# Performance work log

Hardware: AMD Instinct MI355X
Metric: run time of the kernel (lower is better)

The kernel has to match this reference:

```python
import jax, jax.numpy as jnp
import numpy as np


def setup_inputs() -> dict:
    key = jax.random.key(0)
    ks = jax.random.split(key, 5)
    B, S, D, F, E = 4, 4096, 512, 2048, 8
    scale = 0.02
    return {
        "x": jax.random.normal(ks[0], (B, S, D), dtype=jnp.float32),
        "gate_w": jax.random.normal(ks[1], (E, D), dtype=jnp.float32) * scale,
        "w1": jax.random.normal(ks[2], (E, F, D), dtype=jnp.float32) * scale,
        "w2": jax.random.normal(ks[3], (E, D, F), dtype=jnp.float32) * scale,
        "w3": jax.random.normal(ks[4], (E, F, D), dtype=jnp.float32) * scale,
        "top_k": 2,
    }


def _moe(x, gate_w, w1, w2, w3, top_k):
    B, S, D = x.shape
    E = gate_w.shape[0]
    xt = x.reshape(-1, D)                       # [T, D], T = B*S
    T = xt.shape[0]

    # --- router: softmax in float32, top-k, renormalize (matches Mixtral) ---
    logits = xt @ gate_w.T                      # [T, E]
    probs = jax.nn.softmax(logits.astype(jnp.float32), axis=-1)
    rw, sel = jax.lax.top_k(probs, top_k)       # [T, k], [T, k]
    rw = rw / jnp.sum(rw, axis=-1, keepdims=True)
    rw = rw.astype(x.dtype)

    # dense combine weights [T, E]: zero for unselected experts
    combine = jnp.zeros((T, E), dtype=x.dtype)
    combine = combine.at[jnp.arange(T)[:, None], sel].add(rw)

    # --- per-expert SwiGLU-style FFN (relu gate), combined by routing weights ---
    out = jnp.zeros_like(xt)
    for e in range(E):  # small fixed expert count
        h = jax.nn.relu(xt @ w1[e].T) * (xt @ w3[e].T)   # [T, F]
        out = out + combine[:, e:e + 1] * (h @ w2[e].T)  # [T, D]
    return out.reshape(B, S, D)


def reference(x, gate_w, w1, w2, w3, top_k):
    return _moe(x, gate_w, w1, w2, w3, top_k)
```

## Files before the change

kernel.cpp:

```cpp
#include <hip/hip_runtime.h>
#include <stdint.h>

#define T_TOK 16384
#define D_DIM 512
#define F_DIM 2048
#define E_NUM 8
#define MAXR  34816

typedef __bf16 bf16x8 __attribute__((ext_vector_type(8)));
typedef float  f32x4  __attribute__((ext_vector_type(4)));

__device__ __forceinline__ unsigned short f2b(float f) {
  union { float f; unsigned u; } a; a.f = f;
  unsigned u = a.u;
  u = u + 0x7fffu + ((u >> 16) & 1u);
  return (unsigned short)(u >> 16);
}
__device__ __forceinline__ float b2f(unsigned short h) {
  union { unsigned u; float f; } a; a.u = ((unsigned)h) << 16;
  return a.f;
}
__device__ __forceinline__ void load_lds16(const void* g, void* l) {
  __builtin_amdgcn_global_load_lds(
      (const __attribute__((address_space(1))) void*)g,
      (__attribute__((address_space(3))) void*)l, 16, 0, 0);
}

#define CSTRIDE 16

__global__ __launch_bounds__(256) void router_kernel(
    const float* __restrict__ x, const float* __restrict__ gw,
    int* __restrict__ sel, float* __restrict__ rw)
{
  int lane = threadIdx.x & 63;
  int wid  = threadIdx.x >> 6;
  int t = blockIdx.x * 4 + wid;
  const float4* xp = (const float4*)(x + (size_t)t * D_DIM + lane * 8);
  float4 a0 = xp[0], a1 = xp[1];
  float lg[E_NUM];
#pragma unroll
  for (int e = 0; e < E_NUM; ++e) {
    const float4* gp = (const float4*)(gw + (size_t)e * D_DIM + lane * 8);
    float4 g0 = gp[0], g1 = gp[1];
    float s = a0.x*g0.x + a0.y*g0.y + a0.z*g0.z + a0.w*g0.w
            + a1.x*g1.x + a1.y*g1.y + a1.z*g1.z + a1.w*g1.w;
#pragma unroll
    for (int off = 32; off; off >>= 1) s += __shfl_xor(s, off);
    lg[e] = s;
  }
  if (lane == 0) {
    int i0 = 0; float m0 = lg[0];
#pragma unroll
    for (int e = 1; e < E_NUM; ++e) if (lg[e] > m0) { m0 = lg[e]; i0 = e; }
    int i1 = -1; float m1 = -1e30f;
#pragma unroll
    for (int e = 0; e < E_NUM; ++e) if (e != i0 && lg[e] > m1) { m1 = lg[e]; i1 = e; }
    float w0 = 1.0f / (1.0f + expf(m1 - m0));
    sel[2*t] = i0; sel[2*t+1] = i1;
    rw[2*t] = w0;  rw[2*t+1] = 1.0f - w0;
  }
}

__global__ __launch_bounds__(256) void hist_kernel(
    const int* __restrict__ sel, int* __restrict__ counts)
{
  __shared__ int h[E_NUM];
  if (threadIdx.x < E_NUM) h[threadIdx.x] = 0;
  __syncthreads();
  int t = blockIdx.x * 256 + threadIdx.x;
  atomicAdd(&h[sel[2*t]], 1);
  atomicAdd(&h[sel[2*t+1]], 1);
  __syncthreads();
  if (threadIdx.x < E_NUM) atomicAdd(&counts[threadIdx.x * CSTRIDE], h[threadIdx.x]);
}

__global__ void scan_kernel(const int* __restrict__ counts, int* __restrict__ offs,
    int* __restrict__ padTot, int* __restrict__ ptok,
    float* __restrict__ pw, int* __restrict__ pexp)
{
  if (threadIdx.x != 0 || blockIdx.x != 0) return;
  int o = 0;
  for (int e = 0; e < E_NUM; ++e) {
    offs[e] = o;
    int c = counts[e * CSTRIDE];
    int padded = (c + 255) & ~255;
    for (int i = c; i < padded; ++i) { ptok[o+i] = 0; pw[o+i] = 0.0f; pexp[o+i] = e; }
    o += padded;
  }
  *padTot = o;
}

__global__ __launch_bounds__(256) void assign_kernel(
    const int* __restrict__ sel, const float* __restrict__ rw,
    const int* __restrict__ offs, int* __restrict__ cursor,
    int* __restrict__ ptok, float* __restrict__ pw, int* __restrict__ pexp,
    int* __restrict__ t2s)
{
  __shared__ int lcnt[E_NUM];
  __shared__ int base[E_NUM];
  if (threadIdx.x < E_NUM) lcnt[threadIdx.x] = 0;
  __syncthreads();
  int t = blockIdx.x * 256 + threadIdx.x;
  int e[2], rank[2];
  float w[2];
#pragma unroll
  for (int k = 0; k < 2; ++k) {
    e[k] = sel[2*t+k];
    w[k] = rw[2*t+k];
    rank[k] = atomicAdd(&lcnt[e[k]], 1);
  }
  __syncthreads();
  if (threadIdx.x < E_NUM)
    base[threadIdx.x] = atomicAdd(&cursor[threadIdx.x * CSTRIDE], lcnt[threadIdx.x]);
  __syncthreads();
#pragma unroll
  for (int k = 0; k < 2; ++k) {
    int slot = offs[e[k]] + base[e[k]] + rank[k];
    ptok[slot] = t; pw[slot] = w[k]; pexp[slot] = e[k];
    t2s[2*t+k] = slot;
  }
}

__global__ __launch_bounds__(256) void cvt4_kernel(
    const float* __restrict__ s0, const float* __restrict__ s1,
    const float* __restrict__ s2, const float* __restrict__ s3,
    unsigned short* __restrict__ d0, unsigned short* __restrict__ d1,
    unsigned short* __restrict__ d2, unsigned short* __restrict__ d3)
{
  int seg = blockIdx.x >> 13;
  int i = (blockIdx.x & 8191) * 256 + threadIdx.x;
  const float* s = seg == 0 ? s0 : seg == 1 ? s1 : seg == 2 ? s2 : s3;
  unsigned short* d = seg == 0 ? d0 : seg == 1 ? d1 : seg == 2 ? d2 : d3;
  float4 v = ((const float4*)s)[i];
  ushort4 o;
  o.x = f2b(v.x); o.y = f2b(v.y); o.z = f2b(v.z); o.w = f2b(v.w);
  ((ushort4*)d)[i] = o;
}


__device__ __forceinline__ void stageA8(unsigned short* dst, const unsigned short* xb,
    const int* tokr, int kt, int half, int tid, int csw) {
  int k0 = kt * 64;
#pragma unroll
  for (int r = 0; r < 2; ++r) {
    int h = half*2 + r;
    int rl = h*64 + (tid>>3);
    load_lds16(xb + (size_t)tokr[h]*D_DIM + k0 + csw, &dst[rl*64 + (tid&7)*8]);
  }
}
__device__ __forceinline__ void stageB8(unsigned short* dst, const unsigned short* W,
    int f0, int kt, int tid, int csw) {
  int k0 = kt * 64;
#pragma unroll
  for (int r = 0; r < 2; ++r) {
    int rl = r*64 + (tid>>3);
    load_lds16(W + (size_t)(f0+rl)*D_DIM + k0 + csw, &dst[rl*64 + (tid&7)*8]);
  }
}
__device__ __forceinline__ void readA8(bf16x8 (*af)[2], const unsigned short* buf,
    int wm, int lane, int xs, int mlo) {
#pragma unroll
  for (int m = 0; m < 4; ++m)
#pragma unroll
    for (int s = 0; s < 2; ++s)
      af[m][s] = *(const bf16x8*)&buf[(wm*128 + (mlo+m)*16 + (lane&15))*64 + ((s*32 + ((lane>>4)<<3)) ^ xs)];
}
__device__ __forceinline__ void readB8(bf16x8 (*bf)[2], const unsigned short* buf,
    int wn, int lane, int xs) {
#pragma unroll
  for (int n = 0; n < 2; ++n)
#pragma unroll
    for (int s = 0; s < 2; ++s)
      bf[n][s] = *(const bf16x8*)&buf[(wn*32 + n*16 + (lane&15))*64 + ((s*32 + ((lane>>4)<<3)) ^ xs)];
}
__device__ __forceinline__ void mfmaq(f32x4 (*acc)[2], const bf16x8 (*af)[2], const bf16x8 (*bf)[2]) {
#pragma unroll
  for (int m = 0; m < 4; ++m)
#pragma unroll
    for (int n = 0; n < 2; ++n)
#pragma unroll
      for (int s = 0; s < 2; ++s)
        acc[m][n] = __builtin_amdgcn_mfma_f32_16x16x32_bf16(af[m][s], bf[n][s], acc[m][n], 0, 0, 0);
}
#define BAR() __builtin_amdgcn_s_barrier()
#define VMC6() do { asm volatile("s_waitcnt vmcnt(6)" ::: "memory"); \
                    __builtin_amdgcn_sched_barrier(0); } while (0)

__global__ __launch_bounds__(512, 2) void ffn_h8_kernel(
    const unsigned short* __restrict__ xb, const unsigned short* __restrict__ w1b,
    const unsigned short* __restrict__ w3b, const int* __restrict__ ptok,
    const int* __restrict__ pexp, const int* __restrict__ padTot,
    unsigned short* __restrict__ H)
{
  __shared__ unsigned short As0[256*64], As1[256*64];
  __shared__ unsigned short B1s0[128*64], B1s1[128*64];
  __shared__ unsigned short B3s0[128*64], B3s1[128*64];
  int tm = blockIdx.x >> 4;
  int tn = blockIdx.x & 15;
  int row0 = tm * 256;
  if (row0 >= *padTot) return;
  int e  = pexp[row0];
  int f0 = tn * 128;
  const unsigned short* W1 = w1b + (size_t)e * F_DIM * D_DIM;
  const unsigned short* W3 = w3b + (size_t)e * F_DIM * D_DIM;
  int tid  = threadIdx.x;
  int lane = tid & 63;
  int wid  = tid >> 6;
  int wm = wid >> 2, wn = wid & 3;
  int xs  = (lane & 7) << 3;
  int csw = ((tid & 7) ^ ((tid >> 3) & 7)) * 8;

  int tokr[4];
#pragma unroll
  for (int h = 0; h < 4; ++h) tokr[h] = ptok[row0 + h*64 + (tid>>3)];

  f32x4 acc1[8][2] = {};
  f32x4 acc3[8][2] = {};
  bf16x8 afL[4][2], afH[4][2], b1f[2][2], b3f[2][2];

  stageB8(B1s0, W1, f0, 0, tid, csw);
  stageA8(As0, xb, tokr, 0, 0, tid, csw);
  stageA8(As0, xb, tokr, 0, 1, tid, csw);
  stageB8(B3s0, W3, f0, 0, tid, csw);
  stageB8(B1s1, W1, f0, 1, tid, csw);
  stageA8(As1, xb, tokr, 1, 0, tid, csw);
  stageA8(As1, xb, tokr, 1, 1, tid, csw);
  VMC6();
  BAR();

  for (int i = 0; i < 4; ++i) {
    int ktB = 2*i + 1;
    int s2 = (2*i + 2 < 8) ? 2*i + 2 : 6;
    int s3 = (2*i + 3 < 8) ? 2*i + 3 : 7;
    readA8(afL, As0, wm, lane, xs, 0);
    readB8(b1f, B1s0, wn, lane, xs);
    stageB8(B3s1, W3, f0, ktB, tid, csw);
    BAR(); mfmaq(&acc1[0], afL, b1f); BAR();
    readA8(afH, As0, wm, lane, xs, 4);
    stageB8(B1s0, W1, f0, s2, tid, csw);
    BAR(); mfmaq(&acc1[4], afH, b1f); BAR();
    readB8(b3f, B3s0, wn, lane, xs);
    stageA8(As0, xb, tokr, s2, 0, tid, csw);
    BAR(); mfmaq(&acc3[0], afL, b3f); BAR();
    stageA8(As0, xb, tokr, s2, 1, tid, csw);
    VMC6();
    BAR(); mfmaq(&acc3[4], afH, b3f); BAR();
    readA8(afL, As1, wm, lane, xs, 0);
    readB8(b1f, B1s1, wn, lane, xs);
    stageB8(B3s0, W3, f0, s2, tid, csw);
    BAR(); mfmaq(&acc1[0], afL, b1f); BAR();
    readA8(afH, As1, wm, lane, xs, 4);
    stageB8(B1s1, W1, f0, s3, tid, csw);
    BAR(); mfmaq(&acc1[4], afH, b1f); BAR();
    readB8(b3f, B3s1, wn, lane, xs);
    stageA8(As1, xb, tokr, s3, 0, tid, csw);
    BAR(); mfmaq(&acc3[0], afL, b3f); BAR();
    stageA8(As1, xb, tokr, s3, 1, tid, csw);
    VMC6();
    BAR(); mfmaq(&acc3[4], afH, b3f); BAR();
  }

#pragma unroll
  for (int mi = 0; mi < 8; ++mi) {
    int rbase = row0 + wm*128 + mi*16 + (lane>>4)*4;
#pragma unroll
    for (int ni = 0; ni < 2; ++ni) {
      int col = f0 + wn*32 + ni*16 + (lane & 15);
#pragma unroll
      for (int j = 0; j < 4; ++j) {
        float h = fmaxf(acc1[mi][ni][j], 0.0f) * acc3[mi][ni][j];
        H[(size_t)(rbase + j) * F_DIM + col] = f2b(h);
      }
    }
  }
}

__global__ __launch_bounds__(256) void ffn_out_kernel(
    const unsigned short* __restrict__ H, const unsigned short* __restrict__ w2b,
    const int* __restrict__ pexp, const float* __restrict__ pw,
    const int* __restrict__ padTot, unsigned short* __restrict__ contrib)
{
  __shared__ unsigned short As[128 * 64];
  __shared__ unsigned short Bs[128 * 64];
  int tm = blockIdx.x >> 2;
  int tn = blockIdx.x & 3;
  int row0 = tm * 128;
  if (row0 >= *padTot) return;
  int e  = pexp[row0];
  int d0 = tn * 128;
  const unsigned short* W2 = w2b + (size_t)e * D_DIM * F_DIM;
  int lane = threadIdx.x & 63;
  int wid  = threadIdx.x >> 6;
  int wm = wid >> 1, wn = wid & 1;
  int sub  = lane >> 3;
  int colSw = (((lane & 7) ^ sub) * 8);
  int xs = (lane & 7) << 3;

  f32x4 acc[4][4] = {};

  for (int k0 = 0; k0 < F_DIM; k0 += 64) {
#pragma unroll
    for (int c = 0; c < 4; ++c) {
      int r = (wid*4 + c)*8 + sub;
      load_lds16(H  + (size_t)(row0 + r)*F_DIM + k0 + colSw, &As[(wid*4 + c)*512 + lane*8]);
      load_lds16(W2 + (size_t)(d0   + r)*F_DIM + k0 + colSw, &Bs[(wid*4 + c)*512 + lane*8]);
    }
    __syncthreads();
#pragma unroll
    for (int kk = 0; kk < 64; kk += 32) {
      int cphys = (kk + ((lane >> 4) << 3)) ^ xs;
      bf16x8 af[4], bf[4];
#pragma unroll
      for (int mt = 0; mt < 4; ++mt)
        af[mt] = *(const bf16x8*)&As[(wm*64 + mt*16 + (lane&15))*64 + cphys];
#pragma unroll
      for (int nt = 0; nt < 4; ++nt)
        bf[nt] = *(const bf16x8*)&Bs[(wn*64 + nt*16 + (lane&15))*64 + cphys];
#pragma unroll
      for (int mt = 0; mt < 4; ++mt)
#pragma unroll
        for (int nt = 0; nt < 4; ++nt)
          acc[mt][nt] = __builtin_amdgcn_mfma_f32_16x16x32_bf16(af[mt], bf[nt], acc[mt][nt], 0, 0, 0);
    }
    __syncthreads();
  }
#pragma unroll
  for (int mt = 0; mt < 4; ++mt) {
    int rbase = row0 + wm*64 + mt*16 + (lane>>4)*4;
    float sw[4];
#pragma unroll
    for (int j = 0; j < 4; ++j) sw[j] = pw[rbase + j];
#pragma unroll
    for (int nt = 0; nt < 4; ++nt) {
      int col = d0 + wn*64 + nt*16 + (lane & 15);
#pragma unroll
      for (int j = 0; j < 4; ++j)
        contrib[(size_t)(rbase + j) * D_DIM + col] = f2b(acc[mt][nt][j] * sw[j]);
    }
  }
}

__global__ __launch_bounds__(256) void combine_kernel(
    const unsigned short* __restrict__ contrib, const int* __restrict__ t2s,
    float* __restrict__ out)
{
  int i = blockIdx.x * 256 + threadIdx.x;
  int t = i >> 7;
  int c = (i & 127) * 4;
  int s0 = t2s[2*t], s1 = t2s[2*t+1];
  ushort4 u0 = *(const ushort4*)&contrib[(size_t)s0 * D_DIM + c];
  ushort4 u1 = *(const ushort4*)&contrib[(size_t)s1 * D_DIM + c];
  float4 o;
  o.x = b2f(u0.x) + b2f(u1.x);
  o.y = b2f(u0.y) + b2f(u1.y);
  o.z = b2f(u0.z) + b2f(u1.z);
  o.w = b2f(u0.w) + b2f(u1.w);
  *(float4*)&out[(size_t)t * D_DIM + c] = o;
}

#define OFF_SEL   ((size_t)2048)
#define OFF_RW    (OFF_SEL  + (size_t)2*T_TOK*4)
#define OFF_T2S   (OFF_RW   + (size_t)2*T_TOK*4)
#define OFF_PTOK  (OFF_T2S  + (size_t)2*T_TOK*4)
#define OFF_PW    (OFF_PTOK + (size_t)MAXR*4)
#define OFF_PEXP  (OFF_PW   + (size_t)MAXR*4)
#define OFF_XB    (OFF_PEXP + (size_t)MAXR*4)
#define OFF_W1B   (OFF_XB   + (size_t)T_TOK*D_DIM*2)
#define OFF_W3B   (OFF_W1B  + (size_t)E_NUM*F_DIM*D_DIM*2)
#define OFF_W2B   (OFF_W3B  + (size_t)E_NUM*F_DIM*D_DIM*2)
#define OFF_H     (OFF_W2B  + (size_t)E_NUM*F_DIM*D_DIM*2)
#define OFF_CONTR OFF_XB

extern "C" void kernel_launch(void* const* d_in, const int* in_sizes, int n_in,
                              void* d_out, int out_size, void* d_ws, size_t ws_size,
                              hipStream_t stream) {
  const float* x  = (const float*)d_in[0];
  const float* gw = (const float*)d_in[1];
  const float* w1 = (const float*)d_in[2];
  const float* w2 = (const float*)d_in[3];
  const float* w3 = (const float*)d_in[4];
  float* out = (float*)d_out;
  char* ws = (char*)d_ws;

  int*   counts = (int*)(ws + 0);
  int*   cursor = (int*)(ws + 512);
  int*   offs   = (int*)(ws + 1024);
  int*   padTot = (int*)(ws + 1056);
  int*   sel    = (int*)(ws + OFF_SEL);
  float* rw     = (float*)(ws + OFF_RW);
  int*   t2s    = (int*)(ws + OFF_T2S);
  int*   ptok   = (int*)(ws + OFF_PTOK);
  float* pw     = (float*)(ws + OFF_PW);
  int*   pexp   = (int*)(ws + OFF_PEXP);
  unsigned short* xb      = (unsigned short*)(ws + OFF_XB);
  unsigned short* w1b     = (unsigned short*)(ws + OFF_W1B);
  unsigned short* w3b     = (unsigned short*)(ws + OFF_W3B);
  unsigned short* w2b     = (unsigned short*)(ws + OFF_W2B);
  unsigned short* Hbuf    = (unsigned short*)(ws + OFF_H);
  unsigned short* contrib = (unsigned short*)(ws + OFF_CONTR);

  hipMemsetAsync(ws, 0, 2048, stream);

  cvt4_kernel<<<4 * 8192, 256, 0, stream>>>(x, w1, w3, w2, xb, w1b, w3b, w2b);

  router_kernel<<<T_TOK/4, 256, 0, stream>>>(x, gw, sel, rw);
  hist_kernel<<<T_TOK/256, 256, 0, stream>>>(sel, counts);
  scan_kernel<<<1, 64, 0, stream>>>(counts, offs, padTot, ptok, pw, pexp);
  assign_kernel<<<T_TOK/256, 256, 0, stream>>>(sel, rw, offs, cursor, ptok, pw, pexp, t2s);

  ffn_h8_kernel<<<(MAXR/256)*(F_DIM/128), 512, 0, stream>>>(xb, w1b, w3b, ptok, pexp, padTot, Hbuf);
  ffn_out_kernel<<<(MAXR/128)*(D_DIM/128), 256, 0, stream>>>(Hbuf, w2b, pexp, pw, padTot, contrib);
  combine_kernel<<<(T_TOK*D_DIM/4)/256, 256, 0, stream>>>(contrib, t2s, out);

  (void)in_sizes; (void)n_in; (void)out_size; (void)ws_size;
}
```

Measured before the change: 376.7 us.

## Pipeline the down-projection GEMM, parallelize pad fill, remap workgroups per XCD

Replaces the single-buffered down-projection GEMM with a double-buffered, 8-wave pipelined version that uses partial vmcnt waits and raised MFMA priority. It also moves the serial padding fill out of the single-thread scan into a per-expert parallel kernel. Both GEMMs now remap block IDs so consecutive tiles land on the same XCD, which should improve L2 reuse. The new GEMM raises register and LDS use per block, and launches one extra small kernel.

```diff
diff --git a/kernel.cpp b/kernel.cpp
--- a/kernel.cpp
+++ b/kernel.cpp
@@ -27,6 +27,13 @@
 }
 
 #define CSTRIDE 16
+#define BAR() __builtin_amdgcn_s_barrier()
+#define SP1() __builtin_amdgcn_s_setprio(1)
+#define SP0() __builtin_amdgcn_s_setprio(0)
+#define VMC6() do { asm volatile("s_waitcnt vmcnt(6)" ::: "memory"); \
+                    __builtin_amdgcn_sched_barrier(0); } while (0)
+#define VMC2() do { asm volatile("s_waitcnt vmcnt(2)" ::: "memory"); \
+                    __builtin_amdgcn_sched_barrier(0); } while (0)
 
 __global__ __launch_bounds__(256) void router_kernel(
     const float* __restrict__ x, const float* __restrict__ gw,
@@ -75,19 +82,28 @@
 }
 
 __global__ void scan_kernel(const int* __restrict__ counts, int* __restrict__ offs,
-    int* __restrict__ padTot, int* __restrict__ ptok,
-    float* __restrict__ pw, int* __restrict__ pexp)
+    int* __restrict__ padTot)
 {
   if (threadIdx.x != 0 || blockIdx.x != 0) return;
   int o = 0;
   for (int e = 0; e < E_NUM; ++e) {
     offs[e] = o;
-    int c = counts[e * CSTRIDE];
-    int padded = (c + 255) & ~255;
-    for (int i = c; i < padded; ++i) { ptok[o+i] = 0; pw[o+i] = 0.0f; pexp[o+i] = e; }
-    o += padded;
+    o += (counts[e * CSTRIDE] + 255) & ~255;
   }
   *padTot = o;
+}
+
+__global__ __launch_bounds__(256) void padfill_kernel(
+    const int* __restrict__ counts, const int* __restrict__ offs,
+    int* __restrict__ ptok, float* __restrict__ pw, int* __restrict__ pexp)
+{
+  int e = blockIdx.x;
+  int c = counts[e * CSTRIDE];
+  int o = offs[e];
+  int padded = (c + 255) & ~255;
+  for (int i = c + threadIdx.x; i < padded; i += 256) {
+    ptok[o+i] = 0; pw[o+i] = 0.0f; pexp[o+i] = e;
+  }
 }
 
 __global__ __launch_bounds__(256) void assign_kernel(
@@ -174,6 +190,7 @@
       bf[n][s] = *(const bf16x8*)&buf[(wn*32 + n*16 + (lane&15))*64 + ((s*32 + ((lane>>4)<<3)) ^ xs)];
 }
 __device__ __forceinline__ void mfmaq(f32x4 (*acc)[2], const bf16x8 (*af)[2], const bf16x8 (*bf)[2]) {
+  SP1();
 #pragma unroll
   for (int m = 0; m < 4; ++m)
 #pragma unroll
@@ -181,10 +198,8 @@
 #pragma unroll
       for (int s = 0; s < 2; ++s)
         acc[m][n] = __builtin_amdgcn_mfma_f32_16x16x32_bf16(af[m][s], bf[n][s], acc[m][n], 0, 0, 0);
-}
-#define BAR() __builtin_amdgcn_s_barrier()
-#define VMC6() do { asm volatile("s_waitcnt vmcnt(6)" ::: "memory"); \
-                    __builtin_amdgcn_sched_barrier(0); } while (0)
+  SP0();
+}
 
 __global__ __launch_bounds__(512, 2) void ffn_h8_kernel(
     const unsigned short* __restrict__ xb, const unsigned short* __restrict__ w1b,
@@ -195,8 +210,9 @@
   __shared__ unsigned short As0[256*64], As1[256*64];
   __shared__ unsigned short B1s0[128*64], B1s1[128*64];
   __shared__ unsigned short B3s0[128*64], B3s1[128*64];
-  int tm = blockIdx.x >> 4;
-  int tn = blockIdx.x & 15;
+  int wgid = (blockIdx.x & 7) * 272 + (blockIdx.x >> 3);
+  int tm = wgid >> 4;
+  int tn = wgid & 15;
   int row0 = tm * 256;
   if (row0 >= *padTot) return;
   int e  = pexp[row0];
@@ -275,67 +291,113 @@
   }
 }
 
-__global__ __launch_bounds__(256) void ffn_out_kernel(
+__device__ __forceinline__ void stageA_O(unsigned short* dst, const unsigned short* H,
+    int row0, int kt, int tid, int csw) {
+  int k0 = kt * 64;
+#pragma unroll
+  for (int r = 0; r < 2; ++r) {
+    int rl = r*64 + (tid>>3);
+    load_lds16(H + (size_t)(row0+rl)*F_DIM + k0 + csw, &dst[rl*64 + (tid&7)*8]);
+  }
+}
+__device__ __forceinline__ void stageB_O(unsigned short* d1, unsigned short* d3,
+    const unsigned short* W2, int d0, int kt, int tid, int csw) {
+  int k0 = kt * 64;
+  int rl = tid >> 3;
+  load_lds16(W2 + (size_t)(d0+rl)*F_DIM + k0 + csw, &d1[rl*64 + (tid&7)*8]);
+  load_lds16(W2 + (size_t)(d0+64+rl)*F_DIM + k0 + csw, &d3[rl*64 + (tid&7)*8]);
+}
+__device__ __forceinline__ void readA_O(bf16x8 (*af)[2], const unsigned short* buf,
+    int wm, int lane, int xs) {
+#pragma unroll
+  for (int m = 0; m < 4; ++m)
+#pragma unroll
+    for (int s = 0; s < 2; ++s)
+      af[m][s] = *(const bf16x8*)&buf[(wm*64 + m*16 + (lane&15))*64 + ((s*32 + ((lane>>4)<<3)) ^ xs)];
+}
+__device__ __forceinline__ void readB_O(bf16x8* bf, const unsigned short* buf,
+    int wn, int lane, int xs) {
+#pragma unroll
+  for (int s = 0; s < 2; ++s)
+    bf[s] = *(const bf16x8*)&buf[(wn*16 + (lane&15))*64 + ((s*32 + ((lane>>4)<<3)) ^ xs)];
+}
+__device__ __forceinline__ void mfmaO(f32x4* acc, const bf16x8 (*af)[2], const bf16x8* bf) {
+  SP1();
+#pragma unroll
+  for (int m = 0; m < 4; ++m)
+#pragma unroll
+    for (int s = 0; s < 2; ++s)
+      acc[m] = __builtin_amdgcn_mfma_f32_16x16x32_bf16(af[m][s], bf[s], acc[m], 0, 0, 0);
+  SP0();
+}
+
+__global__ __launch_bounds__(512, 4) void ffn_out8_kernel(
     const unsigned short* __restrict__ H, const unsigned short* __restrict__ w2b,
     const int* __restrict__ pexp, const float* __restrict__ pw,
     const int* __restrict__ padTot, unsigned short* __restrict__ contrib)
 {
-  __shared__ unsigned short As[128 * 64];
-  __shared__ unsigned short Bs[128 * 64];
-  int tm = blockIdx.x >> 2;
-  int tn = blockIdx.x & 3;
+  __shared__ unsigned short As0[128*64], As1[128*64];
+  __shared__ unsigned short B1s0[64*64], B1s1[64*64];
+  __shared__ unsigned short B3s0[64*64], B3s1[64*64];
+  int wgid = (blockIdx.x & 7) * 136 + (blockIdx.x >> 3);
+  int tm = wgid >> 2;
+  int tn = wgid & 3;
   int row0 = tm * 128;
   if (row0 >= *padTot) return;
   int e  = pexp[row0];
   int d0 = tn * 128;
   const unsigned short* W2 = w2b + (size_t)e * D_DIM * F_DIM;
-  int lane = threadIdx.x & 63;
-  int wid  = threadIdx.x >> 6;
-  int wm = wid >> 1, wn = wid & 1;
-  int sub  = lane >> 3;
-  int colSw = (((lane & 7) ^ sub) * 8);
-  int xs = (lane & 7) << 3;
-
-  f32x4 acc[4][4] = {};
-
-  for (int k0 = 0; k0 < F_DIM; k0 += 64) {
-#pragma unroll
-    for (int c = 0; c < 4; ++c) {
-      int r = (wid*4 + c)*8 + sub;
-      load_lds16(H  + (size_t)(row0 + r)*F_DIM + k0 + colSw, &As[(wid*4 + c)*512 + lane*8]);
-      load_lds16(W2 + (size_t)(d0   + r)*F_DIM + k0 + colSw, &Bs[(wid*4 + c)*512 + lane*8]);
-    }
-    __syncthreads();
-#pragma unroll
-    for (int kk = 0; kk < 64; kk += 32) {
-      int cphys = (kk + ((lane >> 4) << 3)) ^ xs;
-      bf16x8 af[4], bf[4];
-#pragma unroll
-      for (int mt = 0; mt < 4; ++mt)
-        af[mt] = *(const bf16x8*)&As[(wm*64 + mt*16 + (lane&15))*64 + cphys];
-#pragma unroll
-      for (int nt = 0; nt < 4; ++nt)
-        bf[nt] = *(const bf16x8*)&Bs[(wn*64 + nt*16 + (lane&15))*64 + cphys];
-#pragma unroll
-      for (int mt = 0; mt < 4; ++mt)
-#pragma unroll
-        for (int nt = 0; nt < 4; ++nt)
-          acc[mt][nt] = __builtin_amdgcn_mfma_f32_16x16x32_bf16(af[mt], bf[nt], acc[mt][nt], 0, 0, 0);
-    }
-    __syncthreads();
-  }
-#pragma unroll
-  for (int mt = 0; mt < 4; ++mt) {
-    int rbase = row0 + wm*64 + mt*16 + (lane>>4)*4;
+  int tid  = threadIdx.x;
+  int lane = tid & 63;
+  int wid  = tid >> 6;
+  int wm = wid >> 2, wn = wid & 3;
+  int xs  = (lane & 7) << 3;
+  int csw = ((tid & 7) ^ ((tid >> 3) & 7)) * 8;
+
+  f32x4 acc1[4] = {};
+  f32x4 acc3[4] = {};
+  bf16x8 af[4][2], b1f[2], b3f[2];
+
+  const int NK = F_DIM / 64;
+  stageA_O(As0, H, row0, 0, tid, csw);
+  stageB_O(B1s0, B3s0, W2, d0, 0, tid, csw);
+  stageA_O(As1, H, row0, 1, tid, csw);
+  VMC2();
+  BAR();
+
+  for (int i = 0; i < NK/2; ++i) {
+    int k1 = 2*i + 1;
+    int k2 = (2*i + 2 < NK) ? 2*i + 2 : NK - 1;
+    int k3 = (2*i + 3 < NK) ? 2*i + 3 : NK - 1;
+    readA_O(af, As0, wm, lane, xs);
+    readB_O(b1f, B1s0, wn, lane, xs);
+    readB_O(b3f, B3s0, wn, lane, xs);
+    stageB_O(B1s1, B3s1, W2, d0, k1, tid, csw);
+    BAR(); mfmaO(acc1, af, b1f); BAR();
+    stageA_O(As0, H, row0, k2, tid, csw);
+    VMC2();
+    BAR(); mfmaO(acc3, af, b3f); BAR();
+    readA_O(af, As1, wm, lane, xs);
+    readB_O(b1f, B1s1, wn, lane, xs);
+    readB_O(b3f, B3s1, wn, lane, xs);
+    stageB_O(B1s0, B3s0, W2, d0, k2, tid, csw);
+    BAR(); mfmaO(acc1, af, b1f); BAR();
+    stageA_O(As1, H, row0, k3, tid, csw);
+    VMC2();
+    BAR(); mfmaO(acc3, af, b3f); BAR();
+  }
+
+#pragma unroll
+  for (int m = 0; m < 4; ++m) {
+    int rbase = row0 + wm*64 + m*16 + (lane>>4)*4;
     float sw[4];
 #pragma unroll
     for (int j = 0; j < 4; ++j) sw[j] = pw[rbase + j];
-#pragma unroll
-    for (int nt = 0; nt < 4; ++nt) {
-      int col = d0 + wn*64 + nt*16 + (lane & 15);
-#pragma unroll
-      for (int j = 0; j < 4; ++j)
-        contrib[(size_t)(rbase + j) * D_DIM + col] = f2b(acc[mt][nt][j] * sw[j]);
+    int colL = d0 + wn*16 + (lane & 15);
+#pragma unroll
+    for (int j = 0; j < 4; ++j) {
+      contrib[(size_t)(rbase + j) * D_DIM + colL]      = f2b(acc1[m][j] * sw[j]);
+      contrib[(size_t)(rbase + j) * D_DIM + colL + 64] = f2b(acc3[m][j] * sw[j]);
     }
   }
 }
@@ -405,11 +467,12 @@
 
   router_kernel<<<T_TOK/4, 256, 0, stream>>>(x, gw, sel, rw);
   hist_kernel<<<T_TOK/256, 256, 0, stream>>>(sel, counts);
-  scan_kernel<<<1, 64, 0, stream>>>(counts, offs, padTot, ptok, pw, pexp);
+  scan_kernel<<<1, 64, 0, stream>>>(counts, offs, padTot);
+  padfill_kernel<<<E_NUM, 256, 0, stream>>>(counts, offs, ptok, pw, pexp);
   assign_kernel<<<T_TOK/256, 256, 0, stream>>>(sel, rw, offs, cursor, ptok, pw, pexp, t2s);
 
   ffn_h8_kernel<<<(MAXR/256)*(F_DIM/128), 512, 0, stream>>>(xb, w1b, w3b, ptok, pexp, padTot, Hbuf);
-  ffn_out_kernel<<<(MAXR/128)*(D_DIM/128), 256, 0, stream>>>(Hbuf, w2b, pexp, pw, padTot, contrib);
+  ffn_out8_kernel<<<(MAXR/128)*(D_DIM/128), 512, 0, stream>>>(Hbuf, w2b, pexp, pw, padTot, contrib);
   combine_kernel<<<(T_TOK*D_DIM/4)/256, 256, 0, stream>>>(contrib, t2s, out);
 
   (void)in_sizes; (void)n_in; (void)out_size; (void)ws_size;
```

Result: faster. 331.9 us (-11.9%).
